# Optimization experiments

Measured on AMD Instinct MI355X. Metric: run time of the kernel, lower is better.

## Reference

```python
import jax, jax.numpy as jnp
import numpy as np

EPS = 1e-5

def _conv1x1(x, w, b):
    # x: [B,C,H,W], w: [O,C], b: [O] -> [B,O,H,W]
    return jnp.einsum('bchw,oc->bohw', x, w) + b[None, :, None, None]

def setup_inputs() -> dict:
    key = jax.random.key(0)
    ks = jax.random.split(key, 13)
    B, C, H, W = 16, 256, 64, 64
    Ci = C // 2
    s = 0.05
    return {
        'x': jax.random.normal(ks[0], (B, C, H, W), jnp.float32),
        'g_w': jax.random.normal(ks[1], (Ci, C), jnp.float32) * s,
        'g_b': jax.random.normal(ks[2], (Ci,), jnp.float32) * s,
        'theta_w': jax.random.normal(ks[3], (Ci, C), jnp.float32) * s,
        'theta_b': jax.random.normal(ks[4], (Ci,), jnp.float32) * s,
        'phi_w': jax.random.normal(ks[5], (Ci, C), jnp.float32) * s,
        'phi_b': jax.random.normal(ks[6], (Ci,), jnp.float32) * s,
        'w_w': jax.random.normal(ks[7], (C, Ci), jnp.float32) * s,
        'w_b': jax.random.normal(ks[8], (C,), jnp.float32) * s,
        'bn_gamma': jax.random.normal(ks[9], (C,), jnp.float32),
        'bn_beta': jax.random.normal(ks[10], (C,), jnp.float32),
        'bn_mean': jax.random.normal(ks[11], (C,), jnp.float32),
        'bn_var': jax.random.uniform(ks[12], (C,), jnp.float32, 0.5, 1.5),
    }

def reference(x, g_w, g_b, theta_w, theta_b, phi_w, phi_b,
              w_w, w_b, bn_gamma, bn_beta, bn_mean, bn_var):
    B, C, H, W = x.shape
    N = H * W
    Ci = g_w.shape[0]
    # 1x1 conv projections, flatten spatial to N
    g_x = _conv1x1(x, g_w, g_b).reshape(B, Ci, N).transpose(0, 2, 1)        # [B,N,Ci]
    theta_x = _conv1x1(x, theta_w, theta_b).reshape(B, Ci, N).transpose(0, 2, 1)  # [B,N,Ci]
    phi_x = _conv1x1(x, phi_w, phi_b).reshape(B, Ci, N)                     # [B,Ci,N]
    # affinity f = theta @ phi, normalized by N (softmax-free linear attention)
    f_div_C = jnp.einsum('bnc,bcm->bnm', theta_x, phi_x) / N                # [B,N,N]
    y = jnp.einsum('bnm,bmc->bnc', f_div_C, g_x)                            # [B,N,Ci]
    y = y.transpose(0, 2, 1).reshape(B, Ci, H, W)
    # W: 1x1 conv + BatchNorm (eval mode, running stats)
    w_y = _conv1x1(y, w_w, w_b)
    inv = bn_gamma * jax.lax.rsqrt(bn_var + EPS)
    w_y = w_y * inv[None, :, None, None] + (bn_beta - bn_mean * inv)[None, :, None, None]
    return w_y + x
```

## Files before the change

### kernel.cpp

```cpp
#include <hip/hip_runtime.h>
#include <stdint.h>

#define BATCH 16
#define CH    256
#define CI    128
#define NSP   4096
#define KC    4
#define EPSV  1e-5f

typedef unsigned short u16;
typedef __attribute__((ext_vector_type(4))) float f32x4;
typedef __attribute__((ext_vector_type(8))) short bf16x8;

__device__ __forceinline__ u16 f2b(float f) {
  uint32_t u = __float_as_uint(f);
  uint32_t r = u + 0x7FFFu + ((u >> 16) & 1u);
  return (u16)(r >> 16);
}

__device__ __forceinline__ void async16(void* lds, const void* g) {
  __builtin_amdgcn_global_load_lds(
      (const __attribute__((address_space(1))) unsigned int*)g,
      (__attribute__((address_space(3))) unsigned int*)lds, 16, 0, 0);
}

__global__ __launch_bounds__(256) void k_prep(const float* __restrict__ x,
    u16* __restrict__ xb, u16* __restrict__ xt, float* __restrict__ psum,
    const float* __restrict__ w_w, const float* __restrict__ g_w,
    const float* __restrict__ g_b, const float* __restrict__ theta_w,
    const float* __restrict__ theta_b, const float* __restrict__ phi_w,
    const float* __restrict__ phi_b, const float* __restrict__ w_b,
    const float* __restrict__ bn_g, const float* __restrict__ bn_b,
    const float* __restrict__ bn_m, const float* __restrict__ bn_v,
    float* __restrict__ E, float* __restrict__ KT, float* __restrict__ wg,
    float* __restrict__ tphi, float* __restrict__ q, float* __restrict__ inv,
    float* __restrict__ dconst, float* __restrict__ tb) {
  __shared__ float tile[64*64];
  const int t = threadIdx.x;
  if (blockIdx.z == BATCH) {
    float* lbuf = tile;
    const int id = blockIdx.y*64 + blockIdx.x;
    if (id < 32) {
      const int o0 = id*8;
      #pragma unroll
      for (int k = 0; k < 4; ++k) { int idx = k*256 + t;
        lbuf[idx] = w_w[(size_t)(o0 + (idx & 7))*CI + (idx >> 3)]; }
      __syncthreads();
      float acc[8] = {0.f};
      for (int j = 0; j < CI; ++j) {
        float gv = g_w[(size_t)j*CH + t];
        #pragma unroll
        for (int r = 0; r < 8; ++r) acc[r] += lbuf[j*8 + r] * gv;
      }
      #pragma unroll
      for (int r = 0; r < 8; ++r) E[(size_t)(o0 + r)*CH + t] = acc[r];
    } else if (id < 64) {
      const int a0 = (id - 32)*8;
      #pragma unroll
      for (int k = 0; k < 4; ++k) { int idx = k*256 + t;
        lbuf[idx] = phi_w[(size_t)(idx >> 3)*CH + a0 + (idx & 7)]; }
      __syncthreads();
      float acc[8] = {0.f};
      for (int i = 0; i < CI; ++i) {
        float tv = theta_w[(size_t)i*CH + t];
        #pragma unroll
        for (int u = 0; u < 8; ++u) acc[u] += lbuf[i*8 + u] * tv;
      }
      #pragma unroll
      for (int u = 0; u < 8; ++u) KT[(size_t)(a0 + u)*CH + t] = acc[u];
    } else if (id == 64) {
      float iv = bn_g[t] * rsqrtf(bn_v[t] + EPSV);
      inv[t] = iv;
      dconst[t] = iv*w_b[t] + bn_b[t] - bn_m[t]*iv;
      float a = 0.f;
      for (int j = 0; j < CI; ++j) a += w_w[(size_t)t*CI + j] * g_b[j];
      wg[t] = a;
      float tp = 0.f, qq = 0.f;
      for (int i = 0; i < CI; ++i) {
        tp += theta_w[(size_t)i*CH + t] * phi_b[i];
        qq += phi_w[(size_t)i*CH + t] * theta_b[i];
      }
      tphi[t] = tp; q[t] = qq;
      lbuf[t] = (t < CI) ? theta_b[t]*phi_b[t] : 0.f;
      __syncthreads();
      for (int s2 = 128; s2 > 0; s2 >>= 1) { if (t < s2) lbuf[t] += lbuf[t + s2]; __syncthreads(); }
      if (t == 0) tb[0] = lbuf[0];
    }
    return;
  }
  const int b = blockIdx.z, c0 = blockIdx.y*64, n0 = blockIdx.x*64;
  const int lane16 = t & 15;
  const int grp = t >> 4;
  const float* xp = x + ((size_t)b*CH + c0)*NSP + n0;
  u16* xbp = xb + ((size_t)b*CH + c0)*NSP + n0;
  #pragma unroll
  for (int p = 0; p < 4; ++p) {
    int cl = grp + p*16;
    int nl = lane16*4;
    float4 v = *(const float4*)(xp + (size_t)cl*NSP + nl);
    float ps = v.x + v.y + v.z + v.w;
    #pragma unroll
    for (int o = 1; o < 16; o <<= 1) ps += __shfl_xor(ps, o, 64);
    if (lane16 == 0) psum[((size_t)b*64 + blockIdx.x)*CH + c0 + cl] = ps;
    ushort4 bv; bv.x=f2b(v.x); bv.y=f2b(v.y); bv.z=f2b(v.z); bv.w=f2b(v.w);
    *(ushort4*)(xbp + (size_t)cl*NSP + nl) = bv;
    float vv[4] = {v.x, v.y, v.z, v.w};
    #pragma unroll
    for (int j = 0; j < 4; ++j) {
      int n = nl + j;
      tile[n*64 + (cl ^ (((n>>2)&7)<<2))] = vv[j];
    }
  }
  __syncthreads();
  u16* xtp = xt + ((size_t)b*NSP + n0)*CH + c0;
  #pragma unroll
  for (int q2 = 0; q2 < 4; ++q2) {
    int nl = grp + q2*16;
    int c4 = lane16*4;
    float4 v = *(const float4*)&tile[nl*64 + (c4 ^ (((nl>>2)&7)<<2))];
    ushort4 bv; bv.x=f2b(v.x); bv.y=f2b(v.y); bv.z=f2b(v.z); bv.w=f2b(v.w);
    *(ushort4*)(xtp + (size_t)nl*CH + c4) = bv;
  }
}

__global__ __launch_bounds__(256) void k_gram(const u16* __restrict__ xb, float* __restrict__ Sp) {
  __shared__ u16 As[64*64];
  __shared__ u16 Bs[64*64];
  const int TIa[10] = {0,0,0,0,1,1,1,2,2,3};
  const int TJa[10] = {0,1,2,3,1,2,3,2,3,3};
  const int L = blockIdx.x;
  const int wk = (L & 7) * 80 + (L >> 3);
  const int b = wk / 40;
  const int rem = wk % 40;
  const int kc = rem / 10;
  const int tile = rem % 10;
  const int ti = TIa[tile], tj = TJa[tile];
  const int m_base = ti*64, n_base = tj*64;
  const bool diag = (ti == tj);
  const int t = threadIdx.x, wv = t >> 6, l = t & 63;
  const int wr = wv >> 1, wc = wv & 1;
  const int lr = l & 15, lkb = l >> 4;
  const int sr8 = l >> 3, ss = l & 7;
  const u16* xa = xb + (size_t)b*CH*NSP;
  const int kbeg = kc * (NSP/KC);
  f32x4 acc[2][2];
  #pragma unroll
  for (int i = 0; i < 2; ++i)
    #pragma unroll
    for (int j = 0; j < 2; ++j) acc[i][j] = (f32x4){0.f,0.f,0.f,0.f};

  for (int kk = 0; kk < 16; ++kk) {
    const int kpos = kbeg + kk*64;
    #pragma unroll
    for (int j = 0; j < 2; ++j) {
      const int g = wv*2 + j;
      const int r = g*8 + sr8;
      async16(&As[g*512], xa + (size_t)(m_base + r)*NSP + kpos + ((ss ^ (r & 7)) * 8));
    }
    if (!diag) {
      #pragma unroll
      for (int j = 0; j < 2; ++j) {
        const int g = wv*2 + j;
        const int r = g*8 + sr8;
        async16(&Bs[g*512], xa + (size_t)(n_base + r)*NSP + kpos + ((ss ^ (r & 7)) * 8));
      }
    }
    __syncthreads();
    const u16* bsrc = diag ? As : Bs;
    #pragma unroll
    for (int ks = 0; ks < 2; ++ks) {
      bf16x8 A[2], Bf[2];
      #pragma unroll
      for (int mt = 0; mt < 2; ++mt) {
        const int ra = wr*32 + mt*16 + lr;
        A[mt] = *(const bf16x8*)(As + ra*64 + (((ks*4 + lkb) ^ (ra & 7)) * 8));
      }
      #pragma unroll
      for (int nt = 0; nt < 2; ++nt) {
        const int rb = wc*32 + nt*16 + lr;
        Bf[nt] = *(const bf16x8*)(bsrc + rb*64 + (((ks*4 + lkb) ^ (rb & 7)) * 8));
      }
      #pragma unroll
      for (int mt = 0; mt < 2; ++mt)
        #pragma unroll
        for (int nt = 0; nt < 2; ++nt)
          acc[mt][nt] = __builtin_amdgcn_mfma_f32_16x16x32_bf16(A[mt], Bf[nt], acc[mt][nt], 0, 0, 0);
    }
    __syncthreads();
  }
  float* Sb = Sp + (size_t)((b*KC + kc)*10 + tile)*4096;
  const int r0 = (l >> 4) * 4;
  #pragma unroll
  for (int mt = 0; mt < 2; ++mt)
    #pragma unroll
    for (int nt = 0; nt < 2; ++nt)
      #pragma unroll
      for (int rr = 0; rr < 4; ++rr) {
        const int lm = wr*32 + mt*16 + r0 + rr;
        const int lc = wc*32 + nt*16 + lr;
        Sb[lm*64 + lc] = acc[mt][nt][rr];
      }
}

__global__ __launch_bounds__(256) void k_redvec(const float* __restrict__ Sp,
    const float* __restrict__ psum, const float* __restrict__ E,
    const float* __restrict__ KT, const float* __restrict__ q,
    float* __restrict__ S, float* __restrict__ KS, float* __restrict__ Es,
    float* __restrict__ qs) {
  __shared__ float tl[64*65 + 8];
  const int b = blockIdx.y, xx = blockIdx.x, t = threadIdx.x;
  if (xx < 10) {
    const int TIa[10] = {0,0,0,0,1,1,1,2,2,3};
    const int TJa[10] = {0,1,2,3,1,2,3,2,3,3};
    const int ti = TIa[xx], tj = TJa[xx];
    const int row0 = ti*64, col0 = tj*64;
    float* Sb = S + (size_t)b*CH*CH;
    float4 sum[4];
    #pragma unroll
    for (int k = 0; k < 4; ++k) {
      const int slot = t + k*256;
      const int r = slot >> 4, c4 = (slot & 15) * 4;
      float4 s = {0.f,0.f,0.f,0.f};
      #pragma unroll
      for (int kc = 0; kc < KC; ++kc) {
        const float* p = Sp + (size_t)((b*KC + kc)*10 + xx)*4096;
        float4 v = *(const float4*)(p + r*64 + c4);
        s.x += v.x; s.y += v.y; s.z += v.z; s.w += v.w;
      }
      sum[k] = s;
      *(float4*)(Sb + (size_t)(row0 + r)*CH + col0 + c4) = s;
    }
    if (ti != tj) {
      #pragma unroll
      for (int k = 0; k < 4; ++k) {
        const int slot = t + k*256;
        const int r = slot >> 4, c4 = (slot & 15) * 4;
        tl[r*65 + c4+0] = sum[k].x; tl[r*65 + c4+1] = sum[k].y;
        tl[r*65 + c4+2] = sum[k].z; tl[r*65 + c4+3] = sum[k].w;
      }
      __syncthreads();
      #pragma unroll
      for (int k = 0; k < 4; ++k) {
        const int slot = t + k*256;
        const int r = slot >> 4, c4 = (slot & 15) * 4;
        float4 v = { tl[(c4+0)*65 + r], tl[(c4+1)*65 + r],
                     tl[(c4+2)*65 + r], tl[(c4+3)*65 + r] };
        *(float4*)(Sb + (size_t)(col0 + r)*CH + row0 + c4) = v;
      }
    }
  } else {
    float s = 0.f;
    for (int nb = 0; nb < 64; ++nb) s += psum[((size_t)b*64 + nb)*CH + t];
    tl[t] = s;
    __syncthreads();
    float ks = 0.f;
    for (int a = 0; a < CH; ++a) ks += KT[(size_t)a*CH + t] * tl[a];
    KS[(size_t)b*CH + t] = ks;
    float es = 0.f;
    for (int c = 0; c < CH; ++c) es += E[(size_t)t*CH + c] * tl[c];
    Es[(size_t)b*CH + t] = es;
    float p = q[t] * tl[t];
    #pragma unroll
    for (int o = 1; o < 64; o <<= 1) p += __shfl_xor(p, o, 64);
    if ((t & 63) == 0) tl[4160 + (t >> 6)] = p;
    __syncthreads();
    if (t == 0) qs[b] = tl[4160] + tl[4161] + tl[4162] + tl[4163];
  }
}

__global__ __launch_bounds__(256) void k_RP(const float* __restrict__ S,
    const float* __restrict__ E, const float* __restrict__ KT,
    const float* __restrict__ q, const float* __restrict__ KS,
    const float* __restrict__ Es, const float* __restrict__ qs,
    const float* __restrict__ wg, const float* __restrict__ tphi,
    const float* __restrict__ inv, const float* __restrict__ dconst,
    const float* __restrict__ tb, u16* __restrict__ Pb, float* __restrict__ dv) {
  __shared__ float lEt[2048];
  __shared__ float lRt[2048];
  __shared__ float red[32];
  const int b = blockIdx.y, o0 = blockIdx.x*8, t = threadIdx.x;
  #pragma unroll
  for (int k = 0; k < 8; ++k) { int idx = k*256 + t;
    lEt[idx] = E[(size_t)(o0 + (idx & 7))*CH + (idx >> 3)]; }
  __syncthreads();
  const float* Sb = S + (size_t)b*CH*CH;
  float acc[8] = {0.f};
  for (int c = 0; c < CH; ++c) {
    float sv = Sb[(size_t)c*CH + t];
    #pragma unroll
    for (int r = 0; r < 8; ++r) acc[r] += lEt[c*8 + r] * sv;
  }
  #pragma unroll
  for (int r = 0; r < 8; ++r) lRt[t*8 + r] = acc[r];
  const float qt = q[t];
  #pragma unroll
  for (int r = 0; r < 8; ++r) {
    float p = acc[r] * qt;
    #pragma unroll
    for (int o = 1; o < 64; o <<= 1) p += __shfl_xor(p, o, 64);
    if ((t & 63) == 0) red[r*4 + (t >> 6)] = p;
  }
  __syncthreads();
  float acc2[8] = {0.f};
  for (int a = 0; a < CH; ++a) {
    float kv = KT[(size_t)a*CH + t];
    #pragma unroll
    for (int r = 0; r < 8; ++r) acc2[r] += lRt[a*8 + r] * kv;
  }
  const float ksv = KS[(size_t)b*CH + t], tpv = tphi[t];
  u16* Pbb = Pb + (size_t)b*CH*CH;
  #pragma unroll
  for (int r = 0; r < 8; ++r) {
    int o = o0 + r;
    float val = (acc2[r] + wg[o]*ksv + (Es[(size_t)b*CH + o] + (float)NSP*wg[o])*tpv)
                * inv[o] * (1.f/(float)NSP);
    if (o == t) val += 1.f;
    Pbb[(size_t)o*CH + t] = f2b(val);
  }
  if (t < 8) {
    int o = o0 + t;
    float iv = inv[o], wgo = wg[o], tb0 = tb[0];
    float rq = red[t*4] + red[t*4+1] + red[t*4+2] + red[t*4+3];
    float t2 = rq + wgo*qs[b] + Es[(size_t)b*CH + o]*tb0;
    dv[(size_t)b*CH + o] = iv*(t2*(1.f/(float)NSP) + wgo*tb0) + dconst[o];
  }
}

__global__ __launch_bounds__(512, 4) void k_apply(const u16* __restrict__ Pb,
    const u16* __restrict__ xt, const float* __restrict__ dv,
    float* __restrict__ out) {
  __shared__ union {
    u16   bx[64*256];
    float fe[8][16][68];
  } sm;
  const int b = blockIdx.y, n0 = blockIdx.x*64;
  const int t = threadIdx.x, w = t >> 6, l = t & 63;
  {
    const u16* src = xt + ((size_t)b*NSP + n0)*CH;
    const int r = t >> 3, sbase = t & 7;
    #pragma unroll
    for (int it = 0; it < 4; ++it) {
      int slot = sbase + it*8;
      bf16x8 v = *(const bf16x8*)(src + (size_t)r*CH + slot*8);
      *(bf16x8*)(sm.bx + r*256 + ((slot ^ (r & 7)) * 8)) = v;
    }
  }
  __syncthreads();
  const int m0 = w*32;
  const int lr = l & 15, lkb = l >> 4;
  const int sw = lr & 7;
  const u16* Pp = Pb + (size_t)b*CH*CH;
  f32x4 acc[2][4];
  #pragma unroll
  for (int i = 0; i < 2; ++i)
    #pragma unroll
    for (int j = 0; j < 4; ++j) acc[i][j] = (f32x4){0.f,0.f,0.f,0.f};
  #pragma unroll
  for (int kk = 0; kk < 8; ++kk) {
    bf16x8 A[2], Bf[4];
    #pragma unroll
    for (int mt = 0; mt < 2; ++mt)
      A[mt] = *(const bf16x8*)(Pp + (size_t)(m0 + mt*16 + lr)*CH + kk*32 + lkb*8);
    #pragma unroll
    for (int nt = 0; nt < 4; ++nt) {
      int slot = kk*4 + lkb;
      Bf[nt] = *(const bf16x8*)(sm.bx + (nt*16 + lr)*256 + ((slot ^ sw) * 8));
    }
    #pragma unroll
    for (int mt = 0; mt < 2; ++mt)
      #pragma unroll
      for (int nt = 0; nt < 4; ++nt)
        acc[mt][nt] = __builtin_amdgcn_mfma_f32_16x16x32_bf16(A[mt], Bf[nt], acc[mt][nt], 0, 0, 0);
  }
  __syncthreads();
  float* ob = out + (size_t)b*CH*NSP;
  const int r0 = (l >> 4) * 4;
  #pragma unroll
  for (int mt = 0; mt < 2; ++mt) {
    #pragma unroll
    for (int rr = 0; rr < 4; ++rr) {
      float dval = dv[(size_t)b*CH + m0 + mt*16 + r0 + rr];
      #pragma unroll
      for (int nt = 0; nt < 4; ++nt)
        sm.fe[w][r0 + rr][nt*16 + lr] = acc[mt][nt][rr] + dval;
    }
    #pragma unroll
    for (int i = 0; i < 4; ++i) {
      int s = l + 64*i;
      int rrow = s >> 4, c4 = (s & 15) * 4;
      float4 v = *(const float4*)&sm.fe[w][rrow][c4];
      *(float4*)&ob[(size_t)(m0 + mt*16 + rrow)*NSP + n0 + c4] = v;
    }
  }
}

static constexpr size_t XT_OFF = 0;
static constexpr size_t S_OFF  = 33554432;
static constexpr size_t PB_OFF = 37748736;
static constexpr size_t PS_OFF = 39845888;
static constexpr size_t E_OFF  = 40894464;
static constexpr size_t KT_OFF = 41156608;
static constexpr size_t WG_OFF = 41418752;
static constexpr size_t TP_OFF = 41419776;
static constexpr size_t QV_OFF = 41420800;
static constexpr size_t IV_OFF = 41421824;
static constexpr size_t DC_OFF = 41422848;
static constexpr size_t TB_OFF = 41423872;
static constexpr size_t KS_OFF = 41424896;
static constexpr size_t ES_OFF = 41441280;
static constexpr size_t QS_OFF = 41457664;
static constexpr size_t DV_OFF = 41458688;

extern "C" void kernel_launch(void* const* d_in, const int* in_sizes, int n_in,
                              void* d_out, int out_size, void* d_ws, size_t ws_size,
                              hipStream_t stream) {
  const float* x       = (const float*)d_in[0];
  const float* g_w     = (const float*)d_in[1];
  const float* g_b     = (const float*)d_in[2];
  const float* theta_w = (const float*)d_in[3];
  const float* theta_b = (const float*)d_in[4];
  const float* phi_w   = (const float*)d_in[5];
  const float* phi_b   = (const float*)d_in[6];
  const float* w_w     = (const float*)d_in[7];
  const float* w_b     = (const float*)d_in[8];
  const float* bn_g    = (const float*)d_in[9];
  const float* bn_b    = (const float*)d_in[10];
  const float* bn_m    = (const float*)d_in[11];
  const float* bn_v    = (const float*)d_in[12];
  float* out = (float*)d_out;
  char* ws = (char*)d_ws;
  u16*   XT = (u16*)(ws + XT_OFF);
  float* S  = (float*)(ws + S_OFF);
  u16*   Pb = (u16*)(ws + PB_OFF);
  float* PS = (float*)(ws + PS_OFF);
  float* E  = (float*)(ws + E_OFF);
  float* KT = (float*)(ws + KT_OFF);
  float* WG = (float*)(ws + WG_OFF);
  float* TP = (float*)(ws + TP_OFF);
  float* QV = (float*)(ws + QV_OFF);
  float* IV = (float*)(ws + IV_OFF);
  float* DC = (float*)(ws + DC_OFF);
  float* TB = (float*)(ws + TB_OFF);
  float* KS = (float*)(ws + KS_OFF);
  float* ES = (float*)(ws + ES_OFF);
  float* QS = (float*)(ws + QS_OFF);
  float* DV = (float*)(ws + DV_OFF);
  u16*   Xb = (u16*)d_out;
  float* Sp = (float*)((char*)d_out + 33554432);

  k_prep  <<<dim3(64, 4, BATCH+1),        256, 0, stream>>>(x, Xb, XT, PS,
            w_w, g_w, g_b, theta_w, theta_b, phi_w, phi_b, w_b, bn_g, bn_b, bn_m, bn_v,
            E, KT, WG, TP, QV, IV, DC, TB);
  k_gram  <<<dim3(640),                   256, 0, stream>>>(Xb, Sp);
  k_redvec<<<dim3(11, BATCH),             256, 0, stream>>>(Sp, PS, E, KT, QV, S, KS, ES, QS);
  k_RP    <<<dim3(32, BATCH),             256, 0, stream>>>(S, E, KT, QV, KS, ES, QS, WG, TP, IV, DC, TB, Pb, DV);
  k_apply <<<dim3(NSP/64, BATCH),         512, 0, stream>>>(Pb, XT, DV, out);
}
```

Measured before the change: 121.1 us.

## Split bf16 transpose out of prep kernel into separate k_tr kernel

```diff
diff --git a/kernel.cpp b/kernel.cpp
--- a/kernel.cpp
+++ b/kernel.cpp
@@ -24,8 +24,8 @@
       (__attribute__((address_space(3))) unsigned int*)lds, 16, 0, 0);
 }
 
-__global__ __launch_bounds__(256) void k_prep(const float* __restrict__ x,
-    u16* __restrict__ xb, u16* __restrict__ xt, float* __restrict__ psum,
+__global__ __launch_bounds__(256) void k_prep2(const float* __restrict__ x,
+    u16* __restrict__ xb, float* __restrict__ psum,
     const float* __restrict__ w_w, const float* __restrict__ g_w,
     const float* __restrict__ g_b, const float* __restrict__ theta_w,
     const float* __restrict__ theta_b, const float* __restrict__ phi_w,
@@ -35,10 +35,9 @@
     float* __restrict__ E, float* __restrict__ KT, float* __restrict__ wg,
     float* __restrict__ tphi, float* __restrict__ q, float* __restrict__ inv,
     float* __restrict__ dconst, float* __restrict__ tb) {
-  __shared__ float tile[64*64];
+  __shared__ float lbuf[1024];
   const int t = threadIdx.x;
   if (blockIdx.z == BATCH) {
-    float* lbuf = tile;
     const int id = blockIdx.y*64 + blockIdx.x;
     if (id < 32) {
       const int o0 = id*8;
@@ -89,37 +88,48 @@
     return;
   }
   const int b = blockIdx.z, c0 = blockIdx.y*64, n0 = blockIdx.x*64;
-  const int lane16 = t & 15;
-  const int grp = t >> 4;
-  const float* xp = x + ((size_t)b*CH + c0)*NSP + n0;
-  u16* xbp = xb + ((size_t)b*CH + c0)*NSP + n0;
-  #pragma unroll
-  for (int p = 0; p < 4; ++p) {
-    int cl = grp + p*16;
-    int nl = lane16*4;
-    float4 v = *(const float4*)(xp + (size_t)cl*NSP + nl);
-    float ps = v.x + v.y + v.z + v.w;
-    #pragma unroll
-    for (int o = 1; o < 16; o <<= 1) ps += __shfl_xor(ps, o, 64);
-    if (lane16 == 0) psum[((size_t)b*64 + blockIdx.x)*CH + c0 + cl] = ps;
-    ushort4 bv; bv.x=f2b(v.x); bv.y=f2b(v.y); bv.z=f2b(v.z); bv.w=f2b(v.w);
-    *(ushort4*)(xbp + (size_t)cl*NSP + nl) = bv;
-    float vv[4] = {v.x, v.y, v.z, v.w};
-    #pragma unroll
-    for (int j = 0; j < 4; ++j) {
-      int n = nl + j;
-      tile[n*64 + (cl ^ (((n>>2)&7)<<2))] = vv[j];
-    }
+  const int lane8 = t & 7, rq = t >> 3;
+  const float* xp = x + ((size_t)b*CH + c0)*NSP + n0 + lane8*8;
+  u16* xbp = xb + ((size_t)b*CH + c0)*NSP + n0 + lane8*8;
+  #pragma unroll
+  for (int p = 0; p < 2; ++p) {
+    const int cl = rq + p*32;
+    float4 v0 = *(const float4*)(xp + (size_t)cl*NSP);
+    float4 v1 = *(const float4*)(xp + (size_t)cl*NSP + 4);
+    float ps = v0.x+v0.y+v0.z+v0.w + v1.x+v1.y+v1.z+v1.w;
+    #pragma unroll
+    for (int o = 1; o < 8; o <<= 1) ps += __shfl_xor(ps, o, 64);
+    if (lane8 == 0) psum[((size_t)b*64 + blockIdx.x)*CH + c0 + cl] = ps;
+    bf16x8 bv;
+    bv[0]=(short)f2b(v0.x); bv[1]=(short)f2b(v0.y); bv[2]=(short)f2b(v0.z); bv[3]=(short)f2b(v0.w);
+    bv[4]=(short)f2b(v1.x); bv[5]=(short)f2b(v1.y); bv[6]=(short)f2b(v1.z); bv[7]=(short)f2b(v1.w);
+    *(bf16x8*)(xbp + (size_t)cl*NSP) = bv;
+  }
+}
+
+__global__ __launch_bounds__(256) void k_tr(const u16* __restrict__ xb, u16* __restrict__ xt) {
+  __shared__ u16 tl[64*256];
+  const int b = blockIdx.y, n0 = blockIdx.x*64;
+  const int t = threadIdx.x;
+  const int lane8 = t & 7, rq = t >> 3;
+  const u16* src = xb + (size_t)b*CH*NSP + n0;
+  #pragma unroll
+  for (int p = 0; p < 8; ++p) {
+    const int c = rq + p*32;
+    bf16x8 v = *(const bf16x8*)(src + (size_t)c*NSP + lane8*8);
+    const int cs = c ^ (lane8 << 3);
+    #pragma unroll
+    for (int j = 0; j < 8; ++j)
+      tl[(lane8*8 + j)*256 + cs] = (u16)v[j];
   }
   __syncthreads();
-  u16* xtp = xt + ((size_t)b*NSP + n0)*CH + c0;
-  #pragma unroll
-  for (int q2 = 0; q2 < 4; ++q2) {
-    int nl = grp + q2*16;
-    int c4 = lane16*4;
-    float4 v = *(const float4*)&tile[nl*64 + (c4 ^ (((nl>>2)&7)<<2))];
-    ushort4 bv; bv.x=f2b(v.x); bv.y=f2b(v.y); bv.z=f2b(v.z); bv.w=f2b(v.w);
-    *(ushort4*)(xtp + (size_t)nl*CH + c4) = bv;
+  const int c8 = t & 31, nl = t >> 5;
+  u16* dst = xt + ((size_t)b*NSP + n0)*CH;
+  #pragma unroll
+  for (int p2 = 0; p2 < 8; ++p2) {
+    const int n = p2*8 + nl;
+    bf16x8 v = *(const bf16x8*)(tl + n*256 + ((c8*8) ^ (p2 << 3)));
+    *(bf16x8*)(dst + (size_t)n*CH + c8*8) = v;
   }
 }
 
@@ -448,10 +458,11 @@
   u16*   Xb = (u16*)d_out;
   float* Sp = (float*)((char*)d_out + 33554432);
 
-  k_prep  <<<dim3(64, 4, BATCH+1),        256, 0, stream>>>(x, Xb, XT, PS,
+  k_prep2 <<<dim3(64, 4, BATCH+1),        256, 0, stream>>>(x, Xb, PS,
             w_w, g_w, g_b, theta_w, theta_b, phi_w, phi_b, w_b, bn_g, bn_b, bn_m, bn_v,
             E, KT, WG, TP, QV, IV, DC, TB);
   k_gram  <<<dim3(640),                   256, 0, stream>>>(Xb, Sp);
+  k_tr    <<<dim3(64, BATCH),             256, 0, stream>>>(Xb, XT);
   k_redvec<<<dim3(11, BATCH),             256, 0, stream>>>(Sp, PS, E, KT, QV, S, KS, ES, QS);
   k_RP    <<<dim3(32, BATCH),             256, 0, stream>>>(S, E, KT, QV, KS, ES, QS, WG, TP, IV, DC, TB, Pb, DV);
   k_apply <<<dim3(NSP/64, BATCH),         512, 0, stream>>>(Pb, XT, DV, out);
```

Result: slower. 128.9 us (+6.5%).
